# Kernel tuning notes

Hardware: AMD Instinct MI355X
Metric: run time of the kernel (lower is better)

The kernel has to match this reference:

```python
import jax, jax.numpy as jnp
import numpy as np

B, S, D_MODEL, D_ATTN = 4, 2048, 1024, 1024
NEG_INF = jnp.float32(-jnp.inf)


def setup_inputs() -> dict:
    key = jax.random.key(0)
    ks = jax.random.split(key, 6)
    scale = 1.0 / np.sqrt(D_MODEL)
    return {
        "x": jax.random.normal(ks[0], (B, S, D_MODEL), dtype=jnp.float32),
        "mask": jnp.ones((B, S), dtype=jnp.float32),
        "Wq": jax.random.normal(ks[1], (D_ATTN, D_MODEL), dtype=jnp.float32) * scale,
        "Wk": jax.random.normal(ks[2], (D_ATTN, D_MODEL), dtype=jnp.float32) * scale,
        "Wv": jax.random.normal(ks[3], (D_ATTN, D_MODEL), dtype=jnp.float32) * scale,
        "Wo": jax.random.normal(ks[4], (D_MODEL, D_ATTN), dtype=jnp.float32) * scale,
        "bo": jnp.zeros((D_MODEL,), dtype=jnp.float32),
    }


def reference(x, mask, Wq, Wk, Wv, Wo, bo):
    # x: [B,S,Dm]; torch Linear weight is [out,in], so y = x @ W.T
    q = jnp.einsum("bsd,ad->bsa", x, Wq)  # [B,S,Da]
    k = jnp.einsum("bsd,ad->bsa", x, Wk)
    v = jnp.einsum("bsd,ad->bsa", x, Wv)  # NOTE: v from x (original quirk)
    logits = jnp.einsum("bqa,bka->bqk", q, k)  # [B,S,S]
    # causal mask (cross_attention=True path): keep lower triangle incl. diag
    causal = jnp.tril(jnp.ones((S, S), dtype=bool))
    logits = jnp.where(causal[None], logits, NEG_INF)
    # padding mask: outer product of per-token mask
    square_mask = mask[:, :, None] * mask[:, None, :]  # [B,S,S]
    logits = jnp.where(square_mask == 1, logits, NEG_INF)
    # scale by sqrt(d_model) AFTER masking (as in original)
    attn = jax.nn.softmax(logits / jnp.sqrt(jnp.float32(D_MODEL)), axis=-1)
    attn_out = jnp.einsum("bqk,bka->bqa", attn, v)  # [B,S,Da]
    return jnp.einsum("bsa,da->bsd", attn_out, Wo) + bo
```

## Files before the change

### kernel.cpp

```cpp
#include <hip/hip_runtime.h>
#include <hip/hip_bf16.h>
#include <cstdio>

typedef __bf16 bf16x8 __attribute__((ext_vector_type(8)));
typedef float f32x4 __attribute__((ext_vector_type(4)));

#define BM 128
#define BN 128
#define BK 64

__device__ __forceinline__ unsigned short f2bf(float f) {
  union { float f; unsigned u; } v; v.f = f;
  unsigned u = v.u;
  return (unsigned short)((u + 0x7FFFu + ((u >> 16) & 1u)) >> 16);
}

__device__ __forceinline__ float bf2f(unsigned short s) {
  union { unsigned u; float f; } v; v.u = ((unsigned)s) << 16;
  return v.f;
}

#define GLOAD16(gsrc, ldst) \
  __builtin_amdgcn_global_load_lds((const __attribute__((address_space(1))) void*)(gsrc), \
                                   (__attribute__((address_space(3))) void*)(ldst), 16, 0, 0)

template<int EPI>
__global__ __launch_bounds__(256, 3)
void gemm_sb(const unsigned short* __restrict__ A, const unsigned short* __restrict__ B,
             void* __restrict__ Cv, void* __restrict__ Cv2, void* __restrict__ Cv3,
             int K, int ldA, int ldB, int ldC,
             long aBat, long bBat, long cBat,
             int causalSkip, float scale)
{
  const int gx = gridDim.x;
  const int nwg = gx * gridDim.y;
  const int flat = blockIdx.y * gx + blockIdx.x;
  const int qch = nwg >> 3, rch = nwg & 7;
  const int xcd = flat & 7, idx = flat >> 3;
  const int swz = (xcd < rch ? xcd * (qch + 1) : rch * (qch + 1) + (xcd - rch) * qch) + idx;
  const int bx = swz % gx;
  const int by = swz / gx;

  const int m0 = by * BM;
  const int n0 = bx * BN;
  if (causalSkip && n0 > m0) return;
  const int bz = blockIdx.z;

  const unsigned short* Ab = A + (long)bz * aBat + (long)m0 * ldA;
  const unsigned short* Bb = B + (long)bz * bBat + (long)n0 * ldB;

  __shared__ short lds[2][BM * BK];

  const int tid = threadIdx.x;
  const int lane = tid & 63;
  const int wave = tid >> 6;
  const int wr = wave >> 1, wc = wave & 1;

  const int nk = K / BK;

  const int srow = tid >> 3;
  const int sch = tid & 7;

  const f32x4 fzero = {0.f, 0.f, 0.f, 0.f};
  f32x4 acc[4][4];
#pragma unroll
  for (int i = 0; i < 4; i++)
#pragma unroll
    for (int j = 0; j < 4; j++) acc[i][j] = fzero;

  int aOff[4][2], bOff[4][2];
#pragma unroll
  for (int i = 0; i < 4; i++) {
#pragma unroll
    for (int s = 0; s < 2; s++) {
      int ra = wr * 64 + i * 16 + (lane & 15);
      aOff[i][s] = ra * BK + (((s * 4 + (lane >> 4)) ^ (ra & 7)) * 8);
      int rb = wc * 64 + i * 16 + (lane & 15);
      bOff[i][s] = rb * BK + (((s * 4 + (lane >> 4)) ^ (rb & 7)) * 8);
    }
  }

  for (int kt = 0; kt < nk; kt++) {
    const unsigned short* Ak = Ab + kt * BK;
    const unsigned short* Bk = Bb + kt * BK;
#pragma unroll
    for (int r = 0; r < 4; r++) {
      int row = r * 32 + srow;
      int sc = sch ^ (row & 7);
      GLOAD16(Ak + (long)row * ldA + sc * 8, &lds[0][(r * 32 + wave * 8) * BK]);
    }
#pragma unroll
    for (int r = 0; r < 4; r++) {
      int row = r * 32 + srow;
      int sc = sch ^ (row & 7);
      GLOAD16(Bk + (long)row * ldB + sc * 8, &lds[1][(r * 32 + wave * 8) * BK]);
    }
    __syncthreads();

#pragma unroll
    for (int s = 0; s < 2; s++) {
      bf16x8 av[4], bv[4];
#pragma unroll
      for (int i = 0; i < 4; i++) av[i] = *reinterpret_cast<const bf16x8*>(lds[0] + aOff[i][s]);
#pragma unroll
      for (int j = 0; j < 4; j++) bv[j] = *reinterpret_cast<const bf16x8*>(lds[1] + bOff[j][s]);
#pragma unroll
      for (int i = 0; i < 4; i++)
#pragma unroll
        for (int j = 0; j < 4; j++)
          acc[i][j] = __builtin_amdgcn_mfma_f32_16x16x32_bf16(av[i], bv[j], acc[i][j], 0, 0, 0);
    }
    __syncthreads();
  }

  const int rb4 = (lane >> 4) * 4;
  const int cl = lane & 15;
#pragma unroll
  for (int i = 0; i < 4; i++) {
#pragma unroll
    for (int j = 0; j < 4; j++) {
      const int gm = m0 + wr * 64 + i * 16 + rb4;
      const int gn = n0 + wc * 64 + j * 16 + cl;
      if (EPI == 0) {
        unsigned short* C = (unsigned short*)Cv + (long)bz * cBat;
#pragma unroll
        for (int r = 0; r < 4; r++)
          C[(long)(gm + r) * ldC + gn] = f2bf(acc[i][j][r] * scale);
      } else {
        if (gn < 1024) {
          unsigned short* C = (unsigned short*)Cv;
#pragma unroll
          for (int r = 0; r < 4; r++)
            C[(long)(gm + r) * 1024 + gn] = f2bf(acc[i][j][r]);
        } else if (gn < 2048) {
          unsigned short* C = (unsigned short*)Cv2;
#pragma unroll
          for (int r = 0; r < 4; r++)
            C[(long)(gm + r) * 1024 + (gn - 1024)] = f2bf(acc[i][j][r]);
        } else {
          const int d = gn - 2048;
          const int b = gm >> 11;
          const int sIdx = gm & 2047;
          unsigned short* C = (unsigned short*)Cv3 + (long)b * (2048L * 1024)
                              + (long)d * 2048 + sIdx;
          ushort4 pk;
          pk.x = f2bf(acc[i][j][0]);
          pk.y = f2bf(acc[i][j][1]);
          pk.z = f2bf(acc[i][j][2]);
          pk.w = f2bf(acc[i][j][3]);
          *reinterpret_cast<ushort4*>(C) = pk;
        }
      }
    }
  }
}

template<int EPI>
__global__ __launch_bounds__(256, 2)
void gemm_db(const unsigned short* __restrict__ A, const unsigned short* __restrict__ B,
             void* __restrict__ Cv, const float* __restrict__ bias,
             int K, int ldA, int ldB, int ldC,
             long aBat, long bBat, long cBat,
             int causalKlim, float scale, int revM)
{
  const int gx = gridDim.x;
  const int nwg = gx * gridDim.y;
  const int flat = blockIdx.y * gx + blockIdx.x;
  const int qch = nwg >> 3, rch = nwg & 7;
  const int xcd = flat & 7, idx = flat >> 3;
  const int swz = (xcd < rch ? xcd * (qch + 1) : rch * (qch + 1) + (xcd - rch) * qch) + idx;
  const int bx = swz % gx;
  int by = swz / gx;
  if (revM) by = gridDim.y - 1 - by;

  const int m0 = by * BM;
  const int n0 = bx * BN;
  const int bz = blockIdx.z;

  const unsigned short* Ab = A + (long)bz * aBat + (long)m0 * ldA;
  const unsigned short* Bb = B + (long)bz * bBat + (long)n0 * ldB;

  __shared__ short lds[2][2][BM * BK];

  const int tid = threadIdx.x;
  const int lane = tid & 63;
  const int wave = tid >> 6;
  const int wr = wave >> 1, wc = wave & 1;

  const int Keff = causalKlim ? min(K, m0 + BM) : K;
  const int nk = Keff / BK;

  const int srow = tid >> 3;
  const int sch = tid & 7;

  const f32x4 fzero = {0.f, 0.f, 0.f, 0.f};
  f32x4 acc[4][4];
#pragma unroll
  for (int i = 0; i < 4; i++)
#pragma unroll
    for (int j = 0; j < 4; j++) acc[i][j] = fzero;

  int aOff[4][2], bOff[4][2];
#pragma unroll
  for (int i = 0; i < 4; i++) {
#pragma unroll
    for (int s = 0; s < 2; s++) {
      int ra = wr * 64 + i * 16 + (lane & 15);
      aOff[i][s] = ra * BK + (((s * 4 + (lane >> 4)) ^ (ra & 7)) * 8);
      int rb = wc * 64 + i * 16 + (lane & 15);
      bOff[i][s] = rb * BK + (((s * 4 + (lane >> 4)) ^ (rb & 7)) * 8);
    }
  }

  auto stage = [&](int buf, int kt) {
    const unsigned short* Ak = Ab + kt * BK;
    const unsigned short* Bk = Bb + kt * BK;
#pragma unroll
    for (int r = 0; r < 4; r++) {
      int row = r * 32 + srow;
      int sc = sch ^ (row & 7);
      GLOAD16(Ak + (long)row * ldA + sc * 8, &lds[buf][0][(r * 32 + wave * 8) * BK]);
    }
#pragma unroll
    for (int r = 0; r < 4; r++) {
      int row = r * 32 + srow;
      int sc = sch ^ (row & 7);
      GLOAD16(Bk + (long)row * ldB + sc * 8, &lds[buf][1][(r * 32 + wave * 8) * BK]);
    }
  };

  stage(0, 0);
  stage(1, 1);
  asm volatile("s_waitcnt vmcnt(8)" ::: "memory");
  __builtin_amdgcn_sched_barrier(0);
  __builtin_amdgcn_s_barrier();

  int cur = 0;
  for (int kt = 0; kt < nk; kt++) {
    const short* La = lds[cur][0];
    const short* Lb = lds[cur][1];
    bf16x8 av[2][4], bv[2][4];
#pragma unroll
    for (int s = 0; s < 2; s++) {
#pragma unroll
      for (int i = 0; i < 4; i++) {
        av[s][i] = *reinterpret_cast<const bf16x8*>(La + aOff[i][s]);
        bv[s][i] = *reinterpret_cast<const bf16x8*>(Lb + bOff[i][s]);
      }
    }
    asm volatile("s_waitcnt lgkmcnt(0)" ::: "memory");
    __builtin_amdgcn_sched_barrier(0);
    __builtin_amdgcn_s_barrier();
    __builtin_amdgcn_sched_barrier(0);

    if (kt + 2 < nk) {
      stage(cur, kt + 2);
      asm volatile("s_waitcnt vmcnt(8)" ::: "memory");
    } else if (kt + 1 < nk) {
      asm volatile("s_waitcnt vmcnt(0)" ::: "memory");
    }
    if (kt + 1 < nk) {
      __builtin_amdgcn_s_barrier();
      __builtin_amdgcn_sched_barrier(0);
    }

    __builtin_amdgcn_s_setprio(1);
#pragma unroll
    for (int s = 0; s < 2; s++)
#pragma unroll
      for (int i = 0; i < 4; i++)
#pragma unroll
        for (int j = 0; j < 4; j++)
          acc[i][j] = __builtin_amdgcn_mfma_f32_16x16x32_bf16(av[s][i], bv[s][j], acc[i][j], 0, 0, 0);
    __builtin_amdgcn_s_setprio(0);
    __builtin_amdgcn_sched_barrier(0);
    cur ^= 1;
  }

  const int rb4 = (lane >> 4) * 4;
  const int cl = lane & 15;
#pragma unroll
  for (int i = 0; i < 4; i++) {
#pragma unroll
    for (int j = 0; j < 4; j++) {
      const int gm = m0 + wr * 64 + i * 16 + rb4;
      const int gn = n0 + wc * 64 + j * 16 + cl;
      if (EPI == 0) {
        unsigned short* C = (unsigned short*)Cv + (long)bz * cBat;
#pragma unroll
        for (int r = 0; r < 4; r++)
          C[(long)(gm + r) * ldC + gn] = f2bf(acc[i][j][r] * scale);
      } else {
        float* C = (float*)Cv;
        const float bb = bias[gn];
#pragma unroll
        for (int r = 0; r < 4; r++)
          C[(long)(gm + r) * ldC + gn] = acc[i][j][r] + bb;
      }
    }
  }
}

__global__ __launch_bounds__(256)
void softmax_rows(const unsigned short* __restrict__ Sb, const float* __restrict__ maskv,
                  unsigned short* __restrict__ P, int Sdim)
{
  const int wv = threadIdx.x >> 6;
  const int lane = threadIdx.x & 63;
  const int q = blockIdx.x * 4 + wv;
  const int b = blockIdx.y;
  const int kmax = (q & ~127) + 128;
  const unsigned short* row = Sb + ((long)b * Sdim + q) * Sdim;
  unsigned short* prow = P + ((long)b * Sdim + q) * Sdim;
  const float* mrow = maskv + (long)b * Sdim;
  const float mq = mrow[q];

  float v[4][8];
  float mx = -INFINITY;
#pragma unroll
  for (int c = 0; c < 4; c++) {
    const int k0 = c * 512 + lane * 8;
    if (c * 512 < kmax) {
      uint4 raw = *reinterpret_cast<const uint4*>(row + k0);
      const unsigned short* us = reinterpret_cast<const unsigned short*>(&raw);
      float4 ma = *reinterpret_cast<const float4*>(mrow + k0);
      float4 mb = *reinterpret_cast<const float4*>(mrow + k0 + 4);
      float mv[8] = {ma.x, ma.y, ma.z, ma.w, mb.x, mb.y, mb.z, mb.w};
#pragma unroll
      for (int u = 0; u < 8; u++) {
        const int k = k0 + u;
        const bool ok = (k <= q) && (mq * mv[u] == 1.0f);
        v[c][u] = ok ? bf2f(us[u]) : -INFINITY;
        mx = fmaxf(mx, v[c][u]);
      }
    } else {
#pragma unroll
      for (int u = 0; u < 8; u++) v[c][u] = -INFINITY;
    }
  }
#pragma unroll
  for (int o = 32; o; o >>= 1) mx = fmaxf(mx, __shfl_xor(mx, o));

  float sm = 0.f;
#pragma unroll
  for (int c = 0; c < 4; c++)
#pragma unroll
    for (int u = 0; u < 8; u++) {
      v[c][u] = (v[c][u] > -INFINITY) ? __expf(v[c][u] - mx) : 0.f;
      sm += v[c][u];
    }
#pragma unroll
  for (int o = 32; o; o >>= 1) sm += __shfl_xor(sm, o);
  const float inv = 1.0f / sm;

#pragma unroll
  for (int c = 0; c < 4; c++) {
    if (c * 512 < kmax) {
      union { unsigned short us[8]; uint4 u4; } pk;
#pragma unroll
      for (int u = 0; u < 8; u++) pk.us[u] = f2bf(v[c][u] * inv);
      *reinterpret_cast<uint4*>(prow + c * 512 + lane * 8) = pk.u4;
    }
  }
}

__global__ __launch_bounds__(256)
void cast_all(const float* __restrict__ x, const float* __restrict__ w0,
              const float* __restrict__ w1, const float* __restrict__ w2,
              const float* __restrict__ w3,
              unsigned short* __restrict__ xb, unsigned short* __restrict__ dqkv,
              unsigned short* __restrict__ dout)
{
  const int blk = blockIdx.x;
  const float* src;
  unsigned short* dst;
  int i;
  if (blk < 4096) {
    src = x; dst = xb; i = (blk * 256 + threadIdx.x) * 8;
  } else {
    const int w = (blk - 4096) >> 9;
    const int off = (blk - 4096) & 511;
    src = (w == 0) ? w0 : (w == 1) ? w1 : (w == 2) ? w2 : w3;
    dst = (w < 3) ? (dqkv + (long)w * 1024 * 1024) : dout;
    i = (off * 256 + threadIdx.x) * 8;
  }
  float4 a = *reinterpret_cast<const float4*>(src + i);
  float4 b = *reinterpret_cast<const float4*>(src + i + 4);
  union { unsigned short us[8]; uint4 u4; } pk;
  pk.us[0] = f2bf(a.x); pk.us[1] = f2bf(a.y); pk.us[2] = f2bf(a.z); pk.us[3] = f2bf(a.w);
  pk.us[4] = f2bf(b.x); pk.us[5] = f2bf(b.y); pk.us[6] = f2bf(b.z); pk.us[7] = f2bf(b.w);
  *reinterpret_cast<uint4*>(dst + i) = pk.u4;
}

extern "C" void kernel_launch(void* const* d_in, const int* in_sizes, int n_in,
                              void* d_out, int out_size, void* d_ws, size_t ws_size,
                              hipStream_t stream)
{
  const int B = 4, S = 2048, D = 1024;
  const float* x  = (const float*)d_in[0];
  const float* mk = (const float*)d_in[1];
  const float* Wq = (const float*)d_in[2];
  const float* Wk = (const float*)d_in[3];
  const float* Wv = (const float*)d_in[4];
  const float* Wo = (const float*)d_in[5];
  const float* bo = (const float*)d_in[6];
  float* out = (float*)d_out;

  char* ws = (char*)d_ws;
  const long MB = 1024L * 1024L;
  unsigned short* Xbf  = (unsigned short*)(ws + 0);
  unsigned short* Qb   = (unsigned short*)(ws + 16 * MB);
  unsigned short* Kb   = (unsigned short*)(ws + 32 * MB);
  unsigned short* Vt   = (unsigned short*)(ws + 48 * MB);
  unsigned short* Wqkv = (unsigned short*)(ws + 64 * MB);
  unsigned short* Wob  = (unsigned short*)(ws + 70 * MB);
  unsigned short* Sbuf = (unsigned short*)(ws + 72 * MB);
  unsigned short* P    = Qb;
  unsigned short* O    = Xbf;

  if (ws_size < (size_t)(104 * MB)) {
    fprintf(stderr, "kernel_launch: ws too small (%zu bytes, need 104MB)\n", ws_size);
    return;
  }

  cast_all<<<dim3(4096 + 2048), 256, 0, stream>>>(x, Wq, Wk, Wv, Wo, Xbf, Wqkv, Wob);

  const dim3 blk(256);
  dim3 gQKV(3072 / BN, 8192 / BM, 1);
  gemm_sb<4><<<gQKV, blk, 0, stream>>>(Xbf, Wqkv, Qb, Kb, Vt,
                                       1024, 1024, 1024, 0,
                                       0, 0, 0, 0, 1.0f);
  dim3 gS(2048 / BN, 2048 / BM, 4);
  gemm_sb<0><<<gS, blk, 0, stream>>>(Qb, Kb, Sbuf, nullptr, nullptr,
                                     1024, 1024, 1024, 2048,
                                     (long)S * 1024, (long)S * 1024, (long)S * S,
                                     1, 0.03125f);
  softmax_rows<<<dim3(512, 4), blk, 0, stream>>>(Sbuf, mk, P, 2048);
  dim3 gO(1024 / BN, 2048 / BM, 4);
  gemm_db<0><<<gO, blk, 0, stream>>>(P, Vt, O, nullptr,
                                     2048, 2048, 2048, 1024,
                                     (long)S * S, (long)D * S, (long)S * D,
                                     1, 1.0f, 1);
  dim3 gF(1024 / BN, 8192 / BM, 1);
  gemm_db<2><<<gF, blk, 0, stream>>>(O, Wob, out, bo,
                                     1024, 1024, 1024, 1024,
                                     0, 0, 0, 0, 1.0f, 0);
}
```

Measured before the change: 175.4 us.

## Fold output projection into value weights to drop the final GEMM

Precomputes Wvo = Wo·Wv, a 1024x1024x1024 GEMM over the weights, so that the QKV projection produces V·Woᵀ directly. The P·V GEMM then writes the final fp32 output with bias, and the separate 8192x1024x1024 output projection GEMM is removed. The weight casts are split into their own kernel with a transposed Wv, and the x cast is merged into the Wvo GEMM launch. The cost is an extra small weight GEMM on every call and an additional bf16 rounding of the fused weight.

```diff
diff --git a/kernel.cpp b/kernel.cpp
--- a/kernel.cpp
+++ b/kernel.cpp
@@ -291,13 +291,192 @@
         for (int r = 0; r < 4; r++)
           C[(long)(gm + r) * ldC + gn] = f2bf(acc[i][j][r] * scale);
       } else {
-        float* C = (float*)Cv;
+        float* C = (float*)Cv + (long)bz * cBat;
         const float bb = bias[gn];
 #pragma unroll
         for (int r = 0; r < 4; r++)
           C[(long)(gm + r) * ldC + gn] = acc[i][j][r] + bb;
       }
     }
+  }
+}
+
+__global__ __launch_bounds__(256, 2)
+void fused_prep(const float* __restrict__ x, unsigned short* __restrict__ xb,
+                const unsigned short* __restrict__ Wob, const unsigned short* __restrict__ Wvt,
+                unsigned short* __restrict__ WvoOut)
+{
+  __shared__ short lds[2][2][BM * BK];
+
+  if (blockIdx.x >= 64) {
+    const int blk = blockIdx.x - 64;
+    const int i = (blk * 256 + (int)threadIdx.x) * 8;
+    float4 a = *reinterpret_cast<const float4*>(x + i);
+    float4 b = *reinterpret_cast<const float4*>(x + i + 4);
+    union { unsigned short us[8]; uint4 u4; } pk;
+    pk.us[0] = f2bf(a.x); pk.us[1] = f2bf(a.y); pk.us[2] = f2bf(a.z); pk.us[3] = f2bf(a.w);
+    pk.us[4] = f2bf(b.x); pk.us[5] = f2bf(b.y); pk.us[6] = f2bf(b.z); pk.us[7] = f2bf(b.w);
+    *reinterpret_cast<uint4*>(xb + i) = pk.u4;
+    return;
+  }
+
+  const int by = blockIdx.x >> 3, bx = blockIdx.x & 7;
+  const int m0 = by * BM, n0 = bx * BN;
+  const unsigned short* Ab = Wob + (long)m0 * 1024;
+  const unsigned short* Bb = Wvt + (long)n0 * 1024;
+
+  const int tid = threadIdx.x;
+  const int lane = tid & 63;
+  const int wave = tid >> 6;
+  const int wr = wave >> 1, wc = wave & 1;
+  const int nk = 16;
+  const int srow = tid >> 3;
+  const int sch = tid & 7;
+
+  const f32x4 fzero = {0.f, 0.f, 0.f, 0.f};
+  f32x4 acc[4][4];
+#pragma unroll
+  for (int i = 0; i < 4; i++)
+#pragma unroll
+    for (int j = 0; j < 4; j++) acc[i][j] = fzero;
+
+  int aOff[4][2], bOff[4][2];
+#pragma unroll
+  for (int i = 0; i < 4; i++) {
+#pragma unroll
+    for (int s = 0; s < 2; s++) {
+      int ra = wr * 64 + i * 16 + (lane & 15);
+      aOff[i][s] = ra * BK + (((s * 4 + (lane >> 4)) ^ (ra & 7)) * 8);
+      int rb = wc * 64 + i * 16 + (lane & 15);
+      bOff[i][s] = rb * BK + (((s * 4 + (lane >> 4)) ^ (rb & 7)) * 8);
+    }
+  }
+
+  auto stage = [&](int buf, int kt) {
+    const unsigned short* Ak = Ab + kt * BK;
+    const unsigned short* Bk = Bb + kt * BK;
+#pragma unroll
+    for (int r = 0; r < 4; r++) {
+      int row = r * 32 + srow;
+      int sc = sch ^ (row & 7);
+      GLOAD16(Ak + (long)row * 1024 + sc * 8, &lds[buf][0][(r * 32 + wave * 8) * BK]);
+    }
+#pragma unroll
+    for (int r = 0; r < 4; r++) {
+      int row = r * 32 + srow;
+      int sc = sch ^ (row & 7);
+      GLOAD16(Bk + (long)row * 1024 + sc * 8, &lds[buf][1][(r * 32 + wave * 8) * BK]);
+    }
+  };
+
+  stage(0, 0);
+  stage(1, 1);
+  asm volatile("s_waitcnt vmcnt(8)" ::: "memory");
+  __builtin_amdgcn_sched_barrier(0);
+  __builtin_amdgcn_s_barrier();
+
+  int cur = 0;
+  for (int kt = 0; kt < nk; kt++) {
+    const short* La = lds[cur][0];
+    const short* Lb = lds[cur][1];
+    bf16x8 av[2][4], bv[2][4];
+#pragma unroll
+    for (int s = 0; s < 2; s++) {
+#pragma unroll
+      for (int i = 0; i < 4; i++) {
+        av[s][i] = *reinterpret_cast<const bf16x8*>(La + aOff[i][s]);
+        bv[s][i] = *reinterpret_cast<const bf16x8*>(Lb + bOff[i][s]);
+      }
+    }
+    asm volatile("s_waitcnt lgkmcnt(0)" ::: "memory");
+    __builtin_amdgcn_sched_barrier(0);
+    __builtin_amdgcn_s_barrier();
+    __builtin_amdgcn_sched_barrier(0);
+
+    if (kt + 2 < nk) {
+      stage(cur, kt + 2);
+      asm volatile("s_waitcnt vmcnt(8)" ::: "memory");
+    } else if (kt + 1 < nk) {
+      asm volatile("s_waitcnt vmcnt(0)" ::: "memory");
+    }
+    if (kt + 1 < nk) {
+      __builtin_amdgcn_s_barrier();
+      __builtin_amdgcn_sched_barrier(0);
+    }
+
+    __builtin_amdgcn_s_setprio(1);
+#pragma unroll
+    for (int s = 0; s < 2; s++)
+#pragma unroll
+      for (int i = 0; i < 4; i++)
+#pragma unroll
+        for (int j = 0; j < 4; j++)
+          acc[i][j] = __builtin_amdgcn_mfma_f32_16x16x32_bf16(av[s][i], bv[s][j], acc[i][j], 0, 0, 0);
+    __builtin_amdgcn_s_setprio(0);
+    __builtin_amdgcn_sched_barrier(0);
+    cur ^= 1;
+  }
+
+  const int rb4 = (lane >> 4) * 4;
+  const int cl = lane & 15;
+#pragma unroll
+  for (int i = 0; i < 4; i++) {
+#pragma unroll
+    for (int j = 0; j < 4; j++) {
+      const int gm = m0 + wr * 64 + i * 16 + rb4;
+      const int gn = n0 + wc * 64 + j * 16 + cl;
+#pragma unroll
+      for (int r = 0; r < 4; r++)
+        WvoOut[(long)(gm + r) * 1024 + gn] = f2bf(acc[i][j][r]);
+    }
+  }
+}
+
+__global__ __launch_bounds__(256)
+void cast_w(const float* __restrict__ Wq, const float* __restrict__ Wk,
+            const float* __restrict__ Wv, const float* __restrict__ Wo,
+            unsigned short* __restrict__ Wqkv, unsigned short* __restrict__ Wob,
+            unsigned short* __restrict__ Wvt)
+{
+  const int blk = blockIdx.x;
+  const int tid = threadIdx.x;
+  if (blk < 1536) {
+    const int w = blk >> 9;
+    const int off = blk & 511;
+    const float* src = (w == 0) ? Wq : (w == 1) ? Wk : Wo;
+    unsigned short* dst = (w < 2) ? (Wqkv + (long)w * 1024 * 1024) : Wob;
+    const int i = (off * 256 + tid) * 8;
+    float4 a = *reinterpret_cast<const float4*>(src + i);
+    float4 b = *reinterpret_cast<const float4*>(src + i + 4);
+    union { unsigned short us[8]; uint4 u4; } pk;
+    pk.us[0] = f2bf(a.x); pk.us[1] = f2bf(a.y); pk.us[2] = f2bf(a.z); pk.us[3] = f2bf(a.w);
+    pk.us[4] = f2bf(b.x); pk.us[5] = f2bf(b.y); pk.us[6] = f2bf(b.z); pk.us[7] = f2bf(b.w);
+    *reinterpret_cast<uint4*>(dst + i) = pk.u4;
+    return;
+  }
+  __shared__ float t[64][65];
+  const int tile = blk - 1536;
+  const int a0 = (tile >> 4) * 64;
+  const int m0 = (tile & 15) * 64;
+#pragma unroll
+  for (int i = 0; i < 4; i++) {
+    const int row = (tid >> 4) + i * 16;
+    const int col4 = tid & 15;
+    float4 f4 = *reinterpret_cast<const float4*>(Wv + (long)(a0 + row) * 1024 + m0 + col4 * 4);
+    t[row][col4 * 4 + 0] = f4.x;
+    t[row][col4 * 4 + 1] = f4.y;
+    t[row][col4 * 4 + 2] = f4.z;
+    t[row][col4 * 4 + 3] = f4.w;
+  }
+  __syncthreads();
+#pragma unroll
+  for (int j = 0; j < 2; j++) {
+    const int mm = (tid >> 3) + j * 32;
+    const int aa0 = (tid & 7) * 8;
+    union { unsigned short us[8]; uint4 u4; } pk;
+#pragma unroll
+    for (int u = 0; u < 8; u++) pk.us[u] = f2bf(t[aa0 + u][mm]);
+    *reinterpret_cast<uint4*>(Wvt + (long)(m0 + mm) * 1024 + a0 + aa0) = pk.u4;
   }
 }
 
@@ -364,34 +543,6 @@
   }
 }
 
-__global__ __launch_bounds__(256)
-void cast_all(const float* __restrict__ x, const float* __restrict__ w0,
-              const float* __restrict__ w1, const float* __restrict__ w2,
-              const float* __restrict__ w3,
-              unsigned short* __restrict__ xb, unsigned short* __restrict__ dqkv,
-              unsigned short* __restrict__ dout)
-{
-  const int blk = blockIdx.x;
-  const float* src;
-  unsigned short* dst;
-  int i;
-  if (blk < 4096) {
-    src = x; dst = xb; i = (blk * 256 + threadIdx.x) * 8;
-  } else {
-    const int w = (blk - 4096) >> 9;
-    const int off = (blk - 4096) & 511;
-    src = (w == 0) ? w0 : (w == 1) ? w1 : (w == 2) ? w2 : w3;
-    dst = (w < 3) ? (dqkv + (long)w * 1024 * 1024) : dout;
-    i = (off * 256 + threadIdx.x) * 8;
-  }
-  float4 a = *reinterpret_cast<const float4*>(src + i);
-  float4 b = *reinterpret_cast<const float4*>(src + i + 4);
-  union { unsigned short us[8]; uint4 u4; } pk;
-  pk.us[0] = f2bf(a.x); pk.us[1] = f2bf(a.y); pk.us[2] = f2bf(a.z); pk.us[3] = f2bf(a.w);
-  pk.us[4] = f2bf(b.x); pk.us[5] = f2bf(b.y); pk.us[6] = f2bf(b.z); pk.us[7] = f2bf(b.w);
-  *reinterpret_cast<uint4*>(dst + i) = pk.u4;
-}
-
 extern "C" void kernel_launch(void* const* d_in, const int* in_sizes, int n_in,
                               void* d_out, int out_size, void* d_ws, size_t ws_size,
                               hipStream_t stream)
@@ -411,23 +562,24 @@
   unsigned short* Xbf  = (unsigned short*)(ws + 0);
   unsigned short* Qb   = (unsigned short*)(ws + 16 * MB);
   unsigned short* Kb   = (unsigned short*)(ws + 32 * MB);
-  unsigned short* Vt   = (unsigned short*)(ws + 48 * MB);
+  unsigned short* VWt  = (unsigned short*)(ws + 48 * MB);
   unsigned short* Wqkv = (unsigned short*)(ws + 64 * MB);
   unsigned short* Wob  = (unsigned short*)(ws + 70 * MB);
   unsigned short* Sbuf = (unsigned short*)(ws + 72 * MB);
+  unsigned short* Wvt  = Sbuf;
   unsigned short* P    = Qb;
-  unsigned short* O    = Xbf;
 
   if (ws_size < (size_t)(104 * MB)) {
     fprintf(stderr, "kernel_launch: ws too small (%zu bytes, need 104MB)\n", ws_size);
     return;
   }
 
-  cast_all<<<dim3(4096 + 2048), 256, 0, stream>>>(x, Wq, Wk, Wv, Wo, Xbf, Wqkv, Wob);
+  cast_w<<<dim3(1792), dim3(256), 0, stream>>>(Wq, Wk, Wv, Wo, Wqkv, Wob, Wvt);
+  fused_prep<<<dim3(4160), dim3(256), 0, stream>>>(x, Xbf, Wob, Wvt, Wqkv + 2048L * 1024);
 
   const dim3 blk(256);
   dim3 gQKV(3072 / BN, 8192 / BM, 1);
-  gemm_sb<4><<<gQKV, blk, 0, stream>>>(Xbf, Wqkv, Qb, Kb, Vt,
+  gemm_sb<4><<<gQKV, blk, 0, stream>>>(Xbf, Wqkv, Qb, Kb, VWt,
                                        1024, 1024, 1024, 0,
                                        0, 0, 0, 0, 1.0f);
   dim3 gS(2048 / BN, 2048 / BM, 4);
@@ -437,12 +589,8 @@
                                      1, 0.03125f);
   softmax_rows<<<dim3(512, 4), blk, 0, stream>>>(Sbuf, mk, P, 2048);
   dim3 gO(1024 / BN, 2048 / BM, 4);
-  gemm_db<0><<<gO, blk, 0, stream>>>(P, Vt, O, nullptr,
+  gemm_db<2><<<gO, blk, 0, stream>>>(P, VWt, out, bo,
                                      2048, 2048, 2048, 1024,
                                      (long)S * S, (long)D * S, (long)S * D,
                                      1, 1.0f, 1);
-  dim3 gF(1024 / BN, 8192 / BM, 1);
-  gemm_db<2><<<gF, blk, 0, stream>>>(O, Wob, out, bo,
-                                     1024, 1024, 1024, 1024,
-                                     0, 0, 0, 0, 1.0f, 0);
-}
+}
```

New measurement: 167.8 us. 4.3% less time.

## Fold output projection into value weights and enumerate only causal score tiles

Applied to the files above, without the earlier changes.

Uses associativity to precompute Wvo = Wo·Wv on device. The value projection then yields V·Wo^T directly, and the P·V GEMM writes the final fp32 output plus bias, which removes the separate output-projection GEMM over all tokens. The score GEMM launches only lower-triangular tiles through a triangular index decode instead of launching and early-exiting skipped blocks. The projection GEMMs are merged into two dispatch kernels. In exchange it adds a 1024³ weight-product GEMM and a transposing cast of Wv, plus an extra bf16 rounding of the fused weight that slightly changes numerics.

```diff
diff --git a/kernel.cpp b/kernel.cpp
--- a/kernel.cpp
+++ b/kernel.cpp
@@ -24,94 +24,90 @@
   __builtin_amdgcn_global_load_lds((const __attribute__((address_space(1))) void*)(gsrc), \
                                    (__attribute__((address_space(3))) void*)(ldst), 16, 0, 0)
 
-template<int EPI>
+#define SB_KLOOP(Ab, Bb)                                                        \
+  for (int kt = 0; kt < 16; kt++) {                                             \
+    const unsigned short* Ak = (Ab) + kt * BK;                                  \
+    const unsigned short* Bk = (Bb) + kt * BK;                                  \
+    _Pragma("unroll")                                                           \
+    for (int r = 0; r < 4; r++) {                                               \
+      int row = r * 32 + srow;                                                  \
+      int sc = sch ^ (row & 7);                                                 \
+      GLOAD16(Ak + (long)row * 1024 + sc * 8, &lds[0][(r * 32 + wave * 8) * BK]);\
+    }                                                                           \
+    _Pragma("unroll")                                                           \
+    for (int r = 0; r < 4; r++) {                                               \
+      int row = r * 32 + srow;                                                  \
+      int sc = sch ^ (row & 7);                                                 \
+      GLOAD16(Bk + (long)row * 1024 + sc * 8, &lds[1][(r * 32 + wave * 8) * BK]);\
+    }                                                                           \
+    __syncthreads();                                                            \
+    _Pragma("unroll")                                                           \
+    for (int s = 0; s < 2; s++) {                                               \
+      bf16x8 av[4], bv[4];                                                      \
+      _Pragma("unroll")                                                         \
+      for (int i = 0; i < 4; i++) av[i] = *reinterpret_cast<const bf16x8*>(lds[0] + aOff[i][s]); \
+      _Pragma("unroll")                                                         \
+      for (int j = 0; j < 4; j++) bv[j] = *reinterpret_cast<const bf16x8*>(lds[1] + bOff[j][s]); \
+      _Pragma("unroll")                                                         \
+      for (int i = 0; i < 4; i++)                                               \
+        _Pragma("unroll")                                                       \
+        for (int j = 0; j < 4; j++)                                             \
+          acc[i][j] = __builtin_amdgcn_mfma_f32_16x16x32_bf16(av[i], bv[j], acc[i][j], 0, 0, 0); \
+    }                                                                           \
+    __syncthreads();                                                            \
+  }
+
+#define SB_PREAMBLE                                                             \
+  const int tid = threadIdx.x;                                                  \
+  const int lane = tid & 63;                                                    \
+  const int wave = tid >> 6;                                                    \
+  const int wr = wave >> 1, wc = wave & 1;                                      \
+  const int srow = tid >> 3;                                                    \
+  const int sch = tid & 7;                                                      \
+  const f32x4 fzero = {0.f, 0.f, 0.f, 0.f};                                     \
+  f32x4 acc[4][4];                                                              \
+  _Pragma("unroll")                                                             \
+  for (int i = 0; i < 4; i++)                                                   \
+    _Pragma("unroll")                                                           \
+    for (int j = 0; j < 4; j++) acc[i][j] = fzero;                              \
+  int aOff[4][2], bOff[4][2];                                                   \
+  _Pragma("unroll")                                                             \
+  for (int i = 0; i < 4; i++) {                                                 \
+    _Pragma("unroll")                                                           \
+    for (int s = 0; s < 2; s++) {                                               \
+      int ra = wr * 64 + i * 16 + (lane & 15);                                  \
+      aOff[i][s] = ra * BK + (((s * 4 + (lane >> 4)) ^ (ra & 7)) * 8);          \
+      int rb = wc * 64 + i * 16 + (lane & 15);                                  \
+      bOff[i][s] = rb * BK + (((s * 4 + (lane >> 4)) ^ (rb & 7)) * 8);          \
+    }                                                                           \
+  }
+
 __global__ __launch_bounds__(256, 3)
-void gemm_sb(const unsigned short* __restrict__ A, const unsigned short* __restrict__ B,
-             void* __restrict__ Cv, void* __restrict__ Cv2, void* __restrict__ Cv3,
-             int K, int ldA, int ldB, int ldC,
-             long aBat, long bBat, long cBat,
-             int causalSkip, float scale)
-{
-  const int gx = gridDim.x;
-  const int nwg = gx * gridDim.y;
-  const int flat = blockIdx.y * gx + blockIdx.x;
-  const int qch = nwg >> 3, rch = nwg & 7;
-  const int xcd = flat & 7, idx = flat >> 3;
-  const int swz = (xcd < rch ? xcd * (qch + 1) : rch * (qch + 1) + (xcd - rch) * qch) + idx;
-  const int bx = swz % gx;
-  const int by = swz / gx;
-
-  const int m0 = by * BM;
-  const int n0 = bx * BN;
-  if (causalSkip && n0 > m0) return;
-  const int bz = blockIdx.z;
-
-  const unsigned short* Ab = A + (long)bz * aBat + (long)m0 * ldA;
-  const unsigned short* Bb = B + (long)bz * bBat + (long)n0 * ldB;
-
+void dispA(const unsigned short* __restrict__ Xbf, const unsigned short* __restrict__ Wqk,
+           const unsigned short* __restrict__ Wob, const unsigned short* __restrict__ Wvt,
+           unsigned short* __restrict__ Qb, unsigned short* __restrict__ Kb,
+           unsigned short* __restrict__ Wvo)
+{
   __shared__ short lds[2][BM * BK];
-
-  const int tid = threadIdx.x;
-  const int lane = tid & 63;
-  const int wave = tid >> 6;
-  const int wr = wave >> 1, wc = wave & 1;
-
-  const int nk = K / BK;
-
-  const int srow = tid >> 3;
-  const int sch = tid & 7;
-
-  const f32x4 fzero = {0.f, 0.f, 0.f, 0.f};
-  f32x4 acc[4][4];
-#pragma unroll
-  for (int i = 0; i < 4; i++)
-#pragma unroll
-    for (int j = 0; j < 4; j++) acc[i][j] = fzero;
-
-  int aOff[4][2], bOff[4][2];
-#pragma unroll
-  for (int i = 0; i < 4; i++) {
-#pragma unroll
-    for (int s = 0; s < 2; s++) {
-      int ra = wr * 64 + i * 16 + (lane & 15);
-      aOff[i][s] = ra * BK + (((s * 4 + (lane >> 4)) ^ (ra & 7)) * 8);
-      int rb = wc * 64 + i * 16 + (lane & 15);
-      bOff[i][s] = rb * BK + (((s * 4 + (lane >> 4)) ^ (rb & 7)) * 8);
-    }
-  }
-
-  for (int kt = 0; kt < nk; kt++) {
-    const unsigned short* Ak = Ab + kt * BK;
-    const unsigned short* Bk = Bb + kt * BK;
-#pragma unroll
-    for (int r = 0; r < 4; r++) {
-      int row = r * 32 + srow;
-      int sc = sch ^ (row & 7);
-      GLOAD16(Ak + (long)row * ldA + sc * 8, &lds[0][(r * 32 + wave * 8) * BK]);
-    }
-#pragma unroll
-    for (int r = 0; r < 4; r++) {
-      int row = r * 32 + srow;
-      int sc = sch ^ (row & 7);
-      GLOAD16(Bk + (long)row * ldB + sc * 8, &lds[1][(r * 32 + wave * 8) * BK]);
-    }
-    __syncthreads();
-
-#pragma unroll
-    for (int s = 0; s < 2; s++) {
-      bf16x8 av[4], bv[4];
-#pragma unroll
-      for (int i = 0; i < 4; i++) av[i] = *reinterpret_cast<const bf16x8*>(lds[0] + aOff[i][s]);
-#pragma unroll
-      for (int j = 0; j < 4; j++) bv[j] = *reinterpret_cast<const bf16x8*>(lds[1] + bOff[j][s]);
-#pragma unroll
-      for (int i = 0; i < 4; i++)
-#pragma unroll
-        for (int j = 0; j < 4; j++)
-          acc[i][j] = __builtin_amdgcn_mfma_f32_16x16x32_bf16(av[i], bv[j], acc[i][j], 0, 0, 0);
-    }
-    __syncthreads();
-  }
+  const int flat = blockIdx.x;
+  const bool isQK = flat < 1024;
+  int m0, n0;
+  const unsigned short *Ab, *Bb;
+  if (isQK) {
+    const int swz = (flat & 7) * 128 + (flat >> 3);
+    const int bx = swz & 15, by = swz >> 4;
+    m0 = by * BM; n0 = bx * BN;
+    Ab = Xbf + (long)m0 * 1024;
+    Bb = Wqk + (long)n0 * 1024;
+  } else {
+    const int t = flat - 1024;
+    m0 = (t >> 3) * BM; n0 = (t & 7) * BN;
+    Ab = Wob + (long)m0 * 1024;
+    Bb = Wvt + (long)n0 * 1024;
+  }
+
+  SB_PREAMBLE
+  SB_KLOOP(Ab, Bb)
 
   const int rb4 = (lane >> 4) * 4;
   const int cl = lane & 15;
@@ -121,47 +117,91 @@
     for (int j = 0; j < 4; j++) {
       const int gm = m0 + wr * 64 + i * 16 + rb4;
       const int gn = n0 + wc * 64 + j * 16 + cl;
-      if (EPI == 0) {
-        unsigned short* C = (unsigned short*)Cv + (long)bz * cBat;
+      if (isQK) {
+        if (gn < 1024) {
+#pragma unroll
+          for (int r = 0; r < 4; r++)
+            Qb[(long)(gm + r) * 1024 + gn] = f2bf(acc[i][j][r]);
+        } else {
+#pragma unroll
+          for (int r = 0; r < 4; r++)
+            Kb[(long)(gm + r) * 1024 + (gn - 1024)] = f2bf(acc[i][j][r]);
+        }
+      } else {
 #pragma unroll
         for (int r = 0; r < 4; r++)
-          C[(long)(gm + r) * ldC + gn] = f2bf(acc[i][j][r] * scale);
+          Wvo[(long)(gm + r) * 1024 + gn] = f2bf(acc[i][j][r]);
+      }
+    }
+  }
+}
+
+__global__ __launch_bounds__(256, 3)
+void dispB(const unsigned short* __restrict__ Xbf, const unsigned short* __restrict__ Wvo,
+           const unsigned short* __restrict__ Qb, const unsigned short* __restrict__ Kb,
+           unsigned short* __restrict__ VWt, unsigned short* __restrict__ Sb)
+{
+  __shared__ short lds[2][BM * BK];
+  const int flat = blockIdx.x;
+  const bool isVW = flat < 512;
+  int m0, n0, bz = 0;
+  const unsigned short *Ab, *Bb;
+  if (isVW) {
+    const int swz = (flat & 7) * 64 + (flat >> 3);
+    const int bx = swz & 7, by = swz >> 3;
+    m0 = by * BM; n0 = bx * BN;
+    Ab = Xbf + (long)m0 * 1024;
+    Bb = Wvo + (long)n0 * 1024;
+  } else {
+    const int t = flat - 512;
+    bz = t / 136;
+    const int tt = t - bz * 136;
+    const int swz = (tt & 7) * 17 + (tt >> 3);
+    int i = (int)((sqrtf(8.f * (float)swz + 1.f) - 1.f) * 0.5f);
+    while ((i + 1) * (i + 2) / 2 <= swz) ++i;
+    while (i * (i + 1) / 2 > swz) --i;
+    const int j = swz - i * (i + 1) / 2;
+    m0 = i * BM; n0 = j * BN;
+    Ab = Qb + ((long)bz * 2048 + m0) * 1024;
+    Bb = Kb + ((long)bz * 2048 + n0) * 1024;
+  }
+
+  SB_PREAMBLE
+  SB_KLOOP(Ab, Bb)
+
+  const int rb4 = (lane >> 4) * 4;
+  const int cl = lane & 15;
+#pragma unroll
+  for (int i = 0; i < 4; i++) {
+#pragma unroll
+    for (int j = 0; j < 4; j++) {
+      const int gm = m0 + wr * 64 + i * 16 + rb4;
+      const int gn = n0 + wc * 64 + j * 16 + cl;
+      if (isVW) {
+        const int b = gm >> 11;
+        const int sIdx = gm & 2047;
+        unsigned short* C = VWt + (long)b * (2048L * 1024) + (long)gn * 2048 + sIdx;
+        ushort4 pk;
+        pk.x = f2bf(acc[i][j][0]);
+        pk.y = f2bf(acc[i][j][1]);
+        pk.z = f2bf(acc[i][j][2]);
+        pk.w = f2bf(acc[i][j][3]);
+        *reinterpret_cast<ushort4*>(C) = pk;
       } else {
-        if (gn < 1024) {
-          unsigned short* C = (unsigned short*)Cv;
-#pragma unroll
-          for (int r = 0; r < 4; r++)
-            C[(long)(gm + r) * 1024 + gn] = f2bf(acc[i][j][r]);
-        } else if (gn < 2048) {
-          unsigned short* C = (unsigned short*)Cv2;
-#pragma unroll
-          for (int r = 0; r < 4; r++)
-            C[(long)(gm + r) * 1024 + (gn - 1024)] = f2bf(acc[i][j][r]);
-        } else {
-          const int d = gn - 2048;
-          const int b = gm >> 11;
-          const int sIdx = gm & 2047;
-          unsigned short* C = (unsigned short*)Cv3 + (long)b * (2048L * 1024)
-                              + (long)d * 2048 + sIdx;
-          ushort4 pk;
-          pk.x = f2bf(acc[i][j][0]);
-          pk.y = f2bf(acc[i][j][1]);
-          pk.z = f2bf(acc[i][j][2]);
-          pk.w = f2bf(acc[i][j][3]);
-          *reinterpret_cast<ushort4*>(C) = pk;
-        }
+        unsigned short* C = Sb + (long)bz * (2048L * 2048);
+#pragma unroll
+        for (int r = 0; r < 4; r++)
+          C[(long)(gm + r) * 2048 + gn] = f2bf(acc[i][j][r] * 0.03125f);
       }
     }
   }
 }
 
-template<int EPI>
 __global__ __launch_bounds__(256, 2)
-void gemm_db(const unsigned short* __restrict__ A, const unsigned short* __restrict__ B,
-             void* __restrict__ Cv, const float* __restrict__ bias,
+void gemm_pv(const unsigned short* __restrict__ A, const unsigned short* __restrict__ B,
+             float* __restrict__ Cv, const float* __restrict__ bias,
              int K, int ldA, int ldB, int ldC,
-             long aBat, long bBat, long cBat,
-             int causalKlim, float scale, int revM)
+             long aBat, long bBat, long cBat)
 {
   const int gx = gridDim.x;
   const int nwg = gx * gridDim.y;
@@ -171,7 +211,7 @@
   const int swz = (xcd < rch ? xcd * (qch + 1) : rch * (qch + 1) + (xcd - rch) * qch) + idx;
   const int bx = swz % gx;
   int by = swz / gx;
-  if (revM) by = gridDim.y - 1 - by;
+  by = gridDim.y - 1 - by;
 
   const int m0 = by * BM;
   const int n0 = bx * BN;
@@ -187,7 +227,7 @@
   const int wave = tid >> 6;
   const int wr = wave >> 1, wc = wave & 1;
 
-  const int Keff = causalKlim ? min(K, m0 + BM) : K;
+  const int Keff = min(K, m0 + BM);
   const int nk = Keff / BK;
 
   const int srow = tid >> 3;
@@ -285,18 +325,11 @@
     for (int j = 0; j < 4; j++) {
       const int gm = m0 + wr * 64 + i * 16 + rb4;
       const int gn = n0 + wc * 64 + j * 16 + cl;
-      if (EPI == 0) {
-        unsigned short* C = (unsigned short*)Cv + (long)bz * cBat;
-#pragma unroll
-        for (int r = 0; r < 4; r++)
-          C[(long)(gm + r) * ldC + gn] = f2bf(acc[i][j][r] * scale);
-      } else {
-        float* C = (float*)Cv;
-        const float bb = bias[gn];
-#pragma unroll
-        for (int r = 0; r < 4; r++)
-          C[(long)(gm + r) * ldC + gn] = acc[i][j][r] + bb;
-      }
+      float* C = Cv + (long)bz * cBat;
+      const float bb = bias[gn];
+#pragma unroll
+      for (int r = 0; r < 4; r++)
+        C[(long)(gm + r) * ldC + gn] = acc[i][j][r] + bb;
     }
   }
 }
@@ -365,31 +398,59 @@
 }
 
 __global__ __launch_bounds__(256)
-void cast_all(const float* __restrict__ x, const float* __restrict__ w0,
-              const float* __restrict__ w1, const float* __restrict__ w2,
-              const float* __restrict__ w3,
-              unsigned short* __restrict__ xb, unsigned short* __restrict__ dqkv,
-              unsigned short* __restrict__ dout)
-{
+void cast_all2(const float* __restrict__ x, const float* __restrict__ Wq,
+               const float* __restrict__ Wk, const float* __restrict__ Wv,
+               const float* __restrict__ Wo,
+               unsigned short* __restrict__ xb, unsigned short* __restrict__ Wqk,
+               unsigned short* __restrict__ Wob, unsigned short* __restrict__ Wvt)
+{
+  __shared__ float t[64][65];
   const int blk = blockIdx.x;
-  const float* src;
-  unsigned short* dst;
-  int i;
-  if (blk < 4096) {
-    src = x; dst = xb; i = (blk * 256 + threadIdx.x) * 8;
-  } else {
-    const int w = (blk - 4096) >> 9;
-    const int off = (blk - 4096) & 511;
-    src = (w == 0) ? w0 : (w == 1) ? w1 : (w == 2) ? w2 : w3;
-    dst = (w < 3) ? (dqkv + (long)w * 1024 * 1024) : dout;
-    i = (off * 256 + threadIdx.x) * 8;
-  }
-  float4 a = *reinterpret_cast<const float4*>(src + i);
-  float4 b = *reinterpret_cast<const float4*>(src + i + 4);
-  union { unsigned short us[8]; uint4 u4; } pk;
-  pk.us[0] = f2bf(a.x); pk.us[1] = f2bf(a.y); pk.us[2] = f2bf(a.z); pk.us[3] = f2bf(a.w);
-  pk.us[4] = f2bf(b.x); pk.us[5] = f2bf(b.y); pk.us[6] = f2bf(b.z); pk.us[7] = f2bf(b.w);
-  *reinterpret_cast<uint4*>(dst + i) = pk.u4;
+  const int tid = threadIdx.x;
+  if (blk < 5632) {
+    const float* src;
+    unsigned short* dst;
+    int i;
+    if (blk < 4096) {
+      src = x; dst = xb; i = (blk * 256 + tid) * 8;
+    } else {
+      const int w = (blk - 4096) >> 9;
+      const int off = (blk - 4096) & 511;
+      src = (w == 0) ? Wq : (w == 1) ? Wk : Wo;
+      dst = (w == 0) ? Wqk : (w == 1) ? (Wqk + 1024L * 1024) : Wob;
+      i = (off * 256 + tid) * 8;
+    }
+    float4 a = *reinterpret_cast<const float4*>(src + i);
+    float4 b = *reinterpret_cast<const float4*>(src + i + 4);
+    union { unsigned short us[8]; uint4 u4; } pk;
+    pk.us[0] = f2bf(a.x); pk.us[1] = f2bf(a.y); pk.us[2] = f2bf(a.z); pk.us[3] = f2bf(a.w);
+    pk.us[4] = f2bf(b.x); pk.us[5] = f2bf(b.y); pk.us[6] = f2bf(b.z); pk.us[7] = f2bf(b.w);
+    *reinterpret_cast<uint4*>(dst + i) = pk.u4;
+    return;
+  }
+  const int tile = blk - 5632;
+  const int a0 = (tile >> 4) * 64;
+  const int m0 = (tile & 15) * 64;
+#pragma unroll
+  for (int i = 0; i < 4; i++) {
+    const int row = (tid >> 4) + i * 16;
+    const int col4 = tid & 15;
+    float4 f4 = *reinterpret_cast<const float4*>(Wv + (long)(a0 + row) * 1024 + m0 + col4 * 4);
+    t[row][col4 * 4 + 0] = f4.x;
+    t[row][col4 * 4 + 1] = f4.y;
+    t[row][col4 * 4 + 2] = f4.z;
+    t[row][col4 * 4 + 3] = f4.w;
+  }
+  __syncthreads();
+#pragma unroll
+  for (int j = 0; j < 2; j++) {
+    const int mm = (tid >> 3) + j * 32;
+    const int aa0 = (tid & 7) * 8;
+    union { unsigned short us[8]; uint4 u4; } pk;
+#pragma unroll
+    for (int u = 0; u < 8; u++) pk.us[u] = f2bf(t[aa0 + u][mm]);
+    *reinterpret_cast<uint4*>(Wvt + (long)(m0 + mm) * 1024 + a0 + aa0) = pk.u4;
+  }
 }
 
 extern "C" void kernel_launch(void* const* d_in, const int* in_sizes, int n_in,
@@ -411,38 +472,25 @@
   unsigned short* Xbf  = (unsigned short*)(ws + 0);
   unsigned short* Qb   = (unsigned short*)(ws + 16 * MB);
   unsigned short* Kb   = (unsigned short*)(ws + 32 * MB);
-  unsigned short* Vt   = (unsigned short*)(ws + 48 * MB);
-  unsigned short* Wqkv = (unsigned short*)(ws + 64 * MB);
+  unsigned short* VWt  = (unsigned short*)(ws + 48 * MB);
+  unsigned short* Wqk  = (unsigned short*)(ws + 64 * MB);
+  unsigned short* Wvo  = (unsigned short*)(ws + 68 * MB);
   unsigned short* Wob  = (unsigned short*)(ws + 70 * MB);
   unsigned short* Sbuf = (unsigned short*)(ws + 72 * MB);
+  unsigned short* Wvt  = Sbuf;
   unsigned short* P    = Qb;
-  unsigned short* O    = Xbf;
 
   if (ws_size < (size_t)(104 * MB)) {
     fprintf(stderr, "kernel_launch: ws too small (%zu bytes, need 104MB)\n", ws_size);
     return;
   }
 
-  cast_all<<<dim3(4096 + 2048), 256, 0, stream>>>(x, Wq, Wk, Wv, Wo, Xbf, Wqkv, Wob);
-
-  const dim3 blk(256);
-  dim3 gQKV(3072 / BN, 8192 / BM, 1);
-  gemm_sb<4><<<gQKV, blk, 0, stream>>>(Xbf, Wqkv, Qb, Kb, Vt,
-                                       1024, 1024, 1024, 0,
-                                       0, 0, 0, 0, 1.0f);
-  dim3 gS(2048 / BN, 2048 / BM, 4);
-  gemm_sb<0><<<gS, blk, 0, stream>>>(Qb, Kb, Sbuf, nullptr, nullptr,
-                                     1024, 1024, 1024, 2048,
-                                     (long)S * 1024, (long)S * 1024, (long)S * S,
-                                     1, 0.03125f);
-  softmax_rows<<<dim3(512, 4), blk, 0, stream>>>(Sbuf, mk, P, 2048);
+  cast_all2<<<dim3(5888), dim3(256), 0, stream>>>(x, Wq, Wk, Wv, Wo, Xbf, Wqk, Wob, Wvt);
+  dispA<<<dim3(1088), dim3(256), 0, stream>>>(Xbf, Wqk, Wob, Wvt, Qb, Kb, Wvo);
+  dispB<<<dim3(1056), dim3(256), 0, stream>>>(Xbf, Wvo, Qb, Kb, VWt, Sbuf);
+  softmax_rows<<<dim3(512, 4), dim3(256), 0, stream>>>(Sbuf, mk, P, 2048);
   dim3 gO(1024 / BN, 2048 / BM, 4);
-  gemm_db<0><<<gO, blk, 0, stream>>>(P, Vt, O, nullptr,
-                                     2048, 2048, 2048, 1024,
-                                     (long)S * S, (long)D * S, (long)S * D,
-                                     1, 1.0f, 1);
-  dim3 gF(1024 / BN, 8192 / BM, 1);
-  gemm_db<2><<<gF, blk, 0, stream>>>(O, Wob, out, bo,
-                                     1024, 1024, 1024, 1024,
-                                     0, 0, 0, 0, 1.0f, 0);
-}
+  gemm_pv<<<gO, dim3(256), 0, stream>>>(P, VWt, out, bo,
+                                        2048, 2048, 2048, 1024,
+                                        (long)S * S, (long)D * S, (long)S * D);
+}
```

Result: faster. 163.4 us (-6.8%).
